# Optimization experiments

Hardware: AMD Instinct MI355X
Metric: run time of the kernel (lower is better)

## Reference

```python
import jax, jax.numpy as jnp
import numpy as np

B = 4096
STATE_DIM = 64
OBS_DIM = 32
BASE_DEGREE = 8
TIME_STEPS = 96
EPS = 1e-7


def _degree(t):
    # get_degree: degree_params initialized to linspace(0,1,time_steps); used via .item() (static)
    p = float(t) / (TIME_STEPS - 1)
    scaled = 0.5 * (1.0 + np.sin(2.0 * np.pi * p))
    return BASE_DEGREE + int(2.0 * scaled)


def _cheby_fwd_and_jac(x, coeffs, degree):
    """ChebyKAN forward y[b,o] = sum_{i,d} coeffs[i,o,d] * cos(d*acos(clip(tanh(x[b,i]))))
    plus its analytic per-sample Jacobian J[b,o,i] (replaces the torch autograd loop)."""
    t_raw = jnp.tanh(x)                                   # [B, D]
    t_val = jnp.clip(t_raw, -1.0 + EPS, 1.0 - EPS)
    theta = jnp.arccos(t_val)                             # [B, D]
    dvals = jnp.arange(degree + 1, dtype=x.dtype)         # [deg+1]
    ang = theta[..., None] * dvals                        # [B, D, deg+1]
    cheb = jnp.cos(ang)
    ac = coeffs[..., : degree + 1]                        # [D, D, deg+1]
    y = jnp.einsum('bid,iod->bo', cheb, ac)               # [B, D]
    # d cheb / d x = d*sin(d*theta) * (1 - tanh(x)^2) * mask / sqrt(1 - t_val^2)
    mask = ((t_raw > -1.0 + EPS) & (t_raw < 1.0 - EPS)).astype(x.dtype)
    dtheta_dx = -(1.0 - t_raw * t_raw) * mask / jnp.sqrt(1.0 - t_val * t_val)  # [B, D]
    dcheb_dx = -dvals * jnp.sin(ang) * dtheta_dx[..., None]                    # [B, D, deg+1]
    jac = jnp.einsum('bid,iod->boi', dcheb_dx, ac)        # [B, D, D] = dY_o/dx_i
    return y, jac


def setup_inputs() -> dict:
    key = jax.random.key(0)
    ks = jax.random.split(key, 5)
    obs = jax.random.normal(ks[0], (B, OBS_DIM), jnp.float32)
    prev_state = jax.random.normal(ks[1], (B, STATE_DIM), jnp.float32)
    A = jax.random.normal(ks[2], (B, STATE_DIM, STATE_DIM), jnp.float32)
    prev_cov = A @ A.transpose(0, 2, 1) / STATE_DIM + jnp.eye(STATE_DIM, dtype=jnp.float32)  # SPD
    bound = 1.0 / np.sqrt(STATE_DIM * (BASE_DEGREE + 3))  # kaiming-uniform style
    coeffs = jax.random.uniform(ks[3], (STATE_DIM, STATE_DIM, BASE_DEGREE + 3), jnp.float32, -bound, bound)
    M = jax.random.normal(ks[4], (STATE_DIM, OBS_DIM), jnp.float32)
    q, _ = jnp.linalg.qr(M)                               # orthonormal columns
    obs_matrix = q.T.astype(jnp.float32)                  # [OBS_DIM, STATE_DIM], orthogonal rows
    log_Q_diag = jnp.zeros((STATE_DIM,), jnp.float32)
    log_R_diag = jnp.zeros((OBS_DIM,), jnp.float32)
    return dict(obs=obs, prev_state=prev_state, prev_cov=prev_cov, coeffs=coeffs,
                obs_matrix=obs_matrix, log_Q_diag=log_Q_diag, log_R_diag=log_R_diag, t=10)


def reference(obs, prev_state, prev_cov, coeffs, obs_matrix, log_Q_diag, log_R_diag, t):
    degree = _degree(t)
    state_pred, Fj = _cheby_fwd_and_jac(prev_state, coeffs, degree)   # [B,D], [B,D,D]
    q = jnp.exp(log_Q_diag)                                           # [D]
    r = jnp.exp(log_R_diag)                                           # [O]
    H = obs_matrix                                                    # [O, D]
    # cov_pred = F P F^T + Q
    cov_pred = jnp.einsum('bij,bjk,blk->bil', Fj, prev_cov, Fj) + jnp.diag(q)[None]
    obs_pred = state_pred @ H.T                                       # [B, O]
    residual = obs - obs_pred                                         # [B, O]
    # S = H Pp H^T + R
    S = jnp.einsum('ij,bjk,lk->bil', H, cov_pred, H) + jnp.diag(r)[None]
    S_inv = jnp.linalg.pinv(S)                                        # [B, O, O]
    PHt = jnp.einsum('bij,oj->bio', cov_pred, H)                      # [B, D, O]
    K = jnp.einsum('bio,bop->bip', PHt, S_inv)                        # [B, D, O]
    state_update = state_pred + jnp.einsum('bio,bo->bi', K, residual)
    I_KH = jnp.eye(STATE_DIM, dtype=cov_pred.dtype)[None] - jnp.einsum('bio,oj->bij', K, H)
    # Joseph form: (I-KH) Pp (I-KH)^T + K R K^T
    cov_update = (jnp.einsum('bij,bjk,blk->bil', I_KH, cov_pred, I_KH)
                  + jnp.einsum('bio,o,bjo->bij', K, r, K))
    cov_diag = jnp.diagonal(cov_update, axis1=1, axis2=2)
    return state_update, cov_update, cov_diag
```

## Files before the change

kernel.cpp:

```cpp
#include <hip/hip_runtime.h>
#include <math.h>


typedef float f4 __attribute__((ext_vector_type(4)));
typedef float f32x4 __attribute__((ext_vector_type(4)));
typedef short b16x8 __attribute__((ext_vector_type(8)));
typedef short b16x4 __attribute__((ext_vector_type(4)));

#define EPSC 1e-7f
#define MFMA(a, b, c) __builtin_amdgcn_mfma_f32_16x16x32_bf16(a, b, c, 0, 0, 0)
static constexpr size_t CU_OFF = 4096 * 64;
static constexpr size_t CD_OFF = CU_OFF + 4096ull * 4096;

__device__ __forceinline__ void split2(float x, short &h, short &l) {
  unsigned u = __float_as_uint(x);
  h = (short)(u >> 16);
  float rem = x - __uint_as_float(u & 0xffff0000u);
  l = (short)(__float_as_uint(rem) >> 16);
}

__device__ __forceinline__ void split8v(f4 a, f4 b, b16x8 &hi, b16x8 &lo) {
#pragma unroll
  for (int j = 0; j < 4; ++j) {
    short hh, ll;
    split2(a[j], hh, ll); hi[j] = hh; lo[j] = ll;
    split2(b[j], hh, ll); hi[4 + j] = hh; lo[4 + j] = ll;
  }
}

__global__ __launch_bounds__(256, 3) void kalman_fused(
    const float *__restrict__ obs, const float *__restrict__ prev_state,
    const float *__restrict__ prev_cov, const float *__restrict__ coeffs,
    const float *__restrict__ Hm, const float *__restrict__ logQ,
    const float *__restrict__ logR, const int *__restrict__ tptr,
    float *__restrict__ out) {
  __shared__ __align__(16) unsigned char pool[43008];
  unsigned short *sPh = (unsigned short *)(pool);
  unsigned short *sPl = (unsigned short *)(pool + 9216);
  unsigned short *sFh = (unsigned short *)(pool + 18432);
  unsigned short *sFl = (unsigned short *)(pool + 27648);
  float *sT = (float *)(pool);
  float *sCov = (float *)(pool + 18432);
  float *sPHt = (float *)(pool);
  float *sK = (float *)(pool + 9216);
  float *sS = (float *)(pool + 36864);
  float *ypart = (float *)(pool + 36864);
  float *sy = (float *)(pool + 41472);
  float *sresid = (float *)(pool + 41728);
  float *sq = (float *)(pool + 41856);
  float *sr = (float *)(pool + 42112);
  float *sTv = (float *)(pool + 42240);
  float *sSn = (float *)(pool + 42496);
  float *sDth = (float *)(pool + 42752);

  const int tid = (int)threadIdx.x;
  const int b = (int)blockIdx.x;
  const int w = tid >> 6;
  const int l = tid & 63;
  const int lr = l & 15;
  const int h = l >> 4;

  const int tval = tptr[0];
  const float ang = 6.28318530717958647f * ((float)tval / 95.0f);
  const int D = 9 + (int)(1.0f + sinf(ang));

  {
    const float *Pg = prev_cov + (size_t)b * 4096;
#pragma unroll
    for (int e = 0; e < 4; ++e) {
      const int idx = tid + 256 * e;
      f4 v = *(const f4 *)(Pg + 4 * idx);
      const int r = idx >> 4, c = (idx & 15) * 4;
      b16x4 h4, l4;
#pragma unroll
      for (int j = 0; j < 4; ++j) {
        short hh, ll;
        split2(v[j], hh, ll);
        h4[j] = hh; l4[j] = ll;
      }
      *(b16x4 *)(sPh + r * 72 + c) = h4;
      *(b16x4 *)(sPl + r * 72 + c) = l4;
    }
    if (tid < 64) {
      sq[tid] = expf(logQ[tid]);
      const float x = prev_state[b * 64 + tid];
      const float tr_ = tanhf(x);
      const float tv = fminf(fmaxf(tr_, -1.0f + EPSC), 1.0f - EPSC);
      const float sn = sqrtf(fmaxf(1.0f - tv * tv, 0.0f));
      const float mask = (tr_ > -1.0f + EPSC && tr_ < 1.0f - EPSC) ? 1.0f : 0.0f;
      sTv[tid] = tv;
      sSn[tid] = sn;
      sDth[tid] = -(1.0f - tr_ * tr_) * mask / sn;
    } else if (tid < 96) {
      sr[tid - 64] = expf(logR[tid - 64]);
    }
  }
  __syncthreads();

  {
    const int o = tid & 63, g = tid >> 6;
    float yacc = 0.f;
    float fr[16];
#pragma unroll
    for (int ii = 0; ii < 16; ++ii) {
      const int i = g * 16 + ii;
      const float tv = sTv[i], sn = sSn[i], dth = sDth[i];
      const float *cp = coeffs + (size_t)(i * 64 + o) * 11;
      float cy[11];
#pragma unroll
      for (int d = 0; d < 11; ++d) cy[d] = cp[d];
      if (D < 10) cy[9] = 0.f;
      if (D < 11) cy[10] = 0.f;
      float yac = fmaf(cy[1], tv, cy[0]);
      float wac = cy[1] * sn;
      float cm2 = 1.f, cm1 = tv, sm2 = 0.f, sm1 = sn;
      const float tv2 = 2.f * tv;
#pragma unroll
      for (int d = 2; d <= 10; ++d) {
        const float cc = fmaf(tv2, cm1, -cm2);
        const float ss = fmaf(tv2, sm1, -sm2);
        yac = fmaf(cy[d], cc, yac);
        wac = fmaf(cy[d] * (float)d, ss, wac);
        cm2 = cm1; cm1 = cc; sm2 = sm1; sm1 = ss;
      }
      yacc += yac;
      fr[ii] = -dth * wac;
    }
    b16x8 fh0, fh1, fl0, fl1;
#pragma unroll
    for (int j = 0; j < 8; ++j) {
      short hh, ll;
      split2(fr[j], hh, ll); fh0[j] = hh; fl0[j] = ll;
      split2(fr[8 + j], hh, ll); fh1[j] = hh; fl1[j] = ll;
    }
    *(b16x8 *)(sFh + o * 72 + g * 16) = fh0;
    *(b16x8 *)(sFh + o * 72 + g * 16 + 8) = fh1;
    *(b16x8 *)(sFl + o * 72 + g * 16) = fl0;
    *(b16x8 *)(sFl + o * 72 + g * 16 + 8) = fl1;
    ypart[g * 64 + o] = yacc;
  }
  __syncthreads();
  if (tid < 64)
    sy[tid] = ypart[tid] + ypart[64 + tid] + ypart[128 + tid] + ypart[192 + tid];
  __syncthreads();

  if (tid < 32) {
    float racc = obs[b * 32 + tid];
    const float *Hr = Hm + tid * 64;
#pragma unroll
    for (int s = 0; s < 64; s += 4) {
      f4 hv = *(const f4 *)(Hr + s);
      racc -= hv[0] * sy[s] + hv[1] * sy[s + 1] + hv[2] * sy[s + 2] +
              hv[3] * sy[s + 3];
    }
    sresid[tid] = racc;
  }

  f32x4 accT[4] = {{0.f, 0.f, 0.f, 0.f}, {0.f, 0.f, 0.f, 0.f},
                   {0.f, 0.f, 0.f, 0.f}, {0.f, 0.f, 0.f, 0.f}};
  {
    const int m = 16 * w + lr;
#pragma unroll
    for (int kc = 0; kc < 2; ++kc) {
      const int k = kc * 32 + h * 8;
      b16x8 Ah = *(const b16x8 *)(sFh + m * 72 + k);
      b16x8 Al = *(const b16x8 *)(sFl + m * 72 + k);
#pragma unroll
      for (int t = 0; t < 4; ++t) {
        const int n = t * 16 + lr;
        b16x8 Bh = *(const b16x8 *)(sPh + n * 72 + k);
        b16x8 Bl = *(const b16x8 *)(sPl + n * 72 + k);
        accT[t] = MFMA(Ah, Bh, accT[t]);
        accT[t] = MFMA(Al, Bh, accT[t]);
        accT[t] = MFMA(Ah, Bl, accT[t]);
      }
    }
  }
  __syncthreads();
  {
    const int r0 = 16 * w + h * 4;
#pragma unroll
    for (int t = 0; t < 4; ++t)
#pragma unroll
      for (int j = 0; j < 4; ++j)
        sT[(r0 + j) * 68 + t * 16 + lr] = accT[t][j];
  }

  f32x4 accC[4] = {{0.f, 0.f, 0.f, 0.f}, {0.f, 0.f, 0.f, 0.f},
                   {0.f, 0.f, 0.f, 0.f}, {0.f, 0.f, 0.f, 0.f}};
  {
    const int m = 16 * w + lr;
#pragma unroll
    for (int kc = 0; kc < 2; ++kc) {
      const int k = kc * 32 + h * 8;
      f4 a0 = *(const f4 *)(sT + m * 68 + k);
      f4 a1 = *(const f4 *)(sT + m * 68 + k + 4);
      b16x8 Ah, Al;
      split8v(a0, a1, Ah, Al);
#pragma unroll
      for (int t = 0; t < 4; ++t) {
        const int n = t * 16 + lr;
        b16x8 Bh = *(const b16x8 *)(sFh + n * 72 + k);
        b16x8 Bl = *(const b16x8 *)(sFl + n * 72 + k);
        accC[t] = MFMA(Ah, Bh, accC[t]);
        accC[t] = MFMA(Al, Bh, accC[t]);
        accC[t] = MFMA(Ah, Bl, accC[t]);
      }
    }
  }
  __syncthreads();
  {
    const int r0 = 16 * w + h * 4;
#pragma unroll
    for (int t = 0; t < 4; ++t)
#pragma unroll
      for (int j = 0; j < 4; ++j) {
        const int rr = r0 + j, cc = t * 16 + lr;
        float v = accC[t][j];
        if (rr == cc) v += sq[rr];
        sCov[rr * 68 + cc] = v;
      }
  }

  {
    f32x4 acc[2] = {{0.f, 0.f, 0.f, 0.f}, {0.f, 0.f, 0.f, 0.f}};
    const int m = 16 * w + lr;
#pragma unroll
    for (int kc = 0; kc < 2; ++kc) {
      const int k = kc * 32 + h * 8;
      f4 a0 = *(const f4 *)(sCov + m * 68 + k);
      f4 a1 = *(const f4 *)(sCov + m * 68 + k + 4);
      b16x8 Ah, Al;
      split8v(a0, a1, Ah, Al);
#pragma unroll
      for (int t = 0; t < 2; ++t) {
        const int n = t * 16 + lr;
        const float *Hr = Hm + n * 64 + k;
        f4 b0 = *(const f4 *)(Hr);
        f4 b1 = *(const f4 *)(Hr + 4);
        b16x8 Bh, Bl;
        split8v(b0, b1, Bh, Bl);
        acc[t] = MFMA(Ah, Bh, acc[t]);
        acc[t] = MFMA(Al, Bh, acc[t]);
        acc[t] = MFMA(Ah, Bl, acc[t]);
      }
    }
    const int r0 = 16 * w + h * 4;
#pragma unroll
    for (int t = 0; t < 2; ++t)
#pragma unroll
      for (int j = 0; j < 4; ++j)
        sPHt[(r0 + j) * 36 + t * 16 + lr] = acc[t][j];
  }
  __syncthreads();

  {
    const int tr = w >> 1, tc = w & 1;
    f32x4 acc = {0.f, 0.f, 0.f, 0.f};
    const int m = tr * 16 + lr;
    const int n = tc * 16 + lr;
#pragma unroll
    for (int kc = 0; kc < 2; ++kc) {
      const int k = kc * 32 + h * 8;
      const float *Hr = Hm + m * 64 + k;
      f4 a0 = *(const f4 *)(Hr);
      f4 a1 = *(const f4 *)(Hr + 4);
      b16x8 Ah, Al;
      split8v(a0, a1, Ah, Al);
      f4 b0, b1;
#pragma unroll
      for (int j = 0; j < 4; ++j) b0[j] = sPHt[(k + j) * 36 + n];
#pragma unroll
      for (int j = 0; j < 4; ++j) b1[j] = sPHt[(k + 4 + j) * 36 + n];
      b16x8 Bh, Bl;
      split8v(b0, b1, Bh, Bl);
      acc = MFMA(Ah, Bh, acc);
      acc = MFMA(Al, Bh, acc);
      acc = MFMA(Ah, Bl, acc);
    }
    const int r0 = tr * 16 + h * 4;
#pragma unroll
    for (int j = 0; j < 4; ++j) {
      const int rr = r0 + j, cc = tc * 16 + lr;
      float v = acc[j];
      if (rr == cc) v += sr[rr];
      sS[rr * 36 + cc] = v;
    }
  }
  __syncthreads();

  if (w == 0) {
    const int mr = l >> 1, half = l & 1;
    float s0[16];
    const float *gbase = sS + mr * 36 + half * 16;
    {
      f4 v0 = *(const f4 *)(gbase + 0), v1 = *(const f4 *)(gbase + 4);
      f4 v2 = *(const f4 *)(gbase + 8), v3 = *(const f4 *)(gbase + 12);
#pragma unroll
      for (int j = 0; j < 4; ++j) {
        s0[j] = v0[j]; s0[4 + j] = v1[j]; s0[8 + j] = v2[j]; s0[12 + j] = v3[j];
      }
    }
#pragma unroll
    for (int p = 0; p < 32; ++p) {
      const int ph = p >> 4, pi = p & 15;
      float prow[16];
#pragma unroll
      for (int j = 0; j < 16; ++j) prow[j] = __shfl(s0[j], 2 * p + half, 64);
      const float dpp = __shfl(s0[pi], 2 * p + ph, 64);
      const float d = 1.0f / dpp;
      const float fv = __shfl(s0[pi], (l & 62) + ph, 64);
      if (mr == p) {
#pragma unroll
        for (int j = 0; j < 16; ++j) s0[j] = prow[j] * d;
        if (half == ph) s0[pi] = d;
      } else {
        const float fd = fv * d;
#pragma unroll
        for (int j = 0; j < 16; ++j) s0[j] = fmaf(-fd, prow[j], s0[j]);
        if (half == ph) s0[pi] = -fd;
      }
    }
    float *wbase = sS + mr * 36 + half * 16;
    f4 w0 = {s0[0], s0[1], s0[2], s0[3]};
    f4 w1 = {s0[4], s0[5], s0[6], s0[7]};
    f4 w2 = {s0[8], s0[9], s0[10], s0[11]};
    f4 w3 = {s0[12], s0[13], s0[14], s0[15]};
    *(f4 *)(wbase + 0) = w0;
    *(f4 *)(wbase + 4) = w1;
    *(f4 *)(wbase + 8) = w2;
    *(f4 *)(wbase + 12) = w3;
  }
  __syncthreads();

  {
    f32x4 acc[2] = {{0.f, 0.f, 0.f, 0.f}, {0.f, 0.f, 0.f, 0.f}};
    const int m = 16 * w + lr;
    const int k = h * 8;
    f4 a0 = *(const f4 *)(sPHt + m * 36 + k);
    f4 a1 = *(const f4 *)(sPHt + m * 36 + k + 4);
    b16x8 Ah, Al;
    split8v(a0, a1, Ah, Al);
#pragma unroll
    for (int t = 0; t < 2; ++t) {
      const int n = t * 16 + lr;
      f4 b0 = *(const f4 *)(sS + n * 36 + k);
      f4 b1 = *(const f4 *)(sS + n * 36 + k + 4);
      b16x8 Bh, Bl;
      split8v(b0, b1, Bh, Bl);
      acc[t] = MFMA(Ah, Bh, acc[t]);
      acc[t] = MFMA(Al, Bh, acc[t]);
      acc[t] = MFMA(Ah, Bl, acc[t]);
    }
    const int r0 = 16 * w + h * 4;
#pragma unroll
    for (int t = 0; t < 2; ++t)
#pragma unroll
      for (int j = 0; j < 4; ++j)
        sK[(r0 + j) * 36 + t * 16 + lr] = acc[t][j];
  }
  __syncthreads();

  if (tid < 64) {
    float su = sy[tid];
#pragma unroll
    for (int ob = 0; ob < 32; ob += 4) {
      f4 kv = *(const f4 *)(sK + tid * 36 + ob);
      su += kv[0] * sresid[ob] + kv[1] * sresid[ob + 1] +
            kv[2] * sresid[ob + 2] + kv[3] * sresid[ob + 3];
    }
    out[b * 64 + tid] = su;
  }
  {
    const int m = 16 * w + lr;
    const int k = h * 8;
    f4 a0 = *(const f4 *)(sK + m * 36 + k);
    f4 a1 = *(const f4 *)(sK + m * 36 + k + 4);
    a0 = -a0;
    a1 = -a1;
    b16x8 Ah, Al;
    split8v(a0, a1, Ah, Al);
    const int r0 = 16 * w + h * 4;
    float *outc = out + CU_OFF + (size_t)b * 4096;
#pragma unroll
    for (int t = 0; t < 4; ++t) {
      const int n = t * 16 + lr;
      f4 b0 = *(const f4 *)(sPHt + n * 36 + k);
      f4 b1 = *(const f4 *)(sPHt + n * 36 + k + 4);
      b16x8 Bh, Bl;
      split8v(b0, b1, Bh, Bl);
      f32x4 acc;
#pragma unroll
      for (int j = 0; j < 4; ++j) acc[j] = sCov[(r0 + j) * 68 + n];
      acc = MFMA(Ah, Bh, acc);
      acc = MFMA(Al, Bh, acc);
      acc = MFMA(Ah, Bl, acc);
#pragma unroll
      for (int j = 0; j < 4; ++j) {
        const int rr = r0 + j;
        outc[rr * 64 + n] = acc[j];
        if (rr == n) out[CD_OFF + b * 64 + rr] = acc[j];
      }
    }
  }
}

extern "C" void kernel_launch(void *const *d_in, const int *in_sizes, int n_in,
                              void *d_out, int out_size, void *d_ws,
                              size_t ws_size, hipStream_t stream) {
  const float *obs = (const float *)d_in[0];
  const float *prev_state = (const float *)d_in[1];
  const float *prev_cov = (const float *)d_in[2];
  const float *coeffs = (const float *)d_in[3];
  const float *Hm = (const float *)d_in[4];
  const float *logQ = (const float *)d_in[5];
  const float *logR = (const float *)d_in[6];
  const int *tptr = (const int *)d_in[7];
  (void)in_sizes; (void)n_in; (void)out_size; (void)d_ws; (void)ws_size;
  kalman_fused<<<dim3(4096), dim3(256), 0, stream>>>(
      obs, prev_state, prev_cov, coeffs, Hm, logQ, logR, tptr, (float *)d_out);
}
```

Baseline: 128.6 us.

## Store intermediates as packed bf16 hi/lo pairs with XOR-swizzled LDS layout

Intermediate matrices (T, cov_pred, PHt, K) are now stored in LDS as packed 32-bit hi|lo bf16 split words, so consumers unpack them with byte-permute instructions instead of re-splitting floats. Padded row strides are replaced by XOR swizzles to avoid bank conflicts, which shrinks LDS use and lets launch bounds ask for 4 blocks per CU instead of 3. Coefficient loads are vectorized into f4 loads. Risks: storing cov_pred as hi+lo bf16 loses a few mantissa bits in the Joseph-form accumulator input, and higher occupancy may force register spills.

```diff
diff --git a/kernel.cpp b/kernel.cpp
--- a/kernel.cpp
+++ b/kernel.cpp
@@ -6,6 +6,9 @@
 typedef float f32x4 __attribute__((ext_vector_type(4)));
 typedef short b16x8 __attribute__((ext_vector_type(8)));
 typedef short b16x4 __attribute__((ext_vector_type(4)));
+typedef unsigned int u32;
+typedef unsigned int u32x4 __attribute__((ext_vector_type(4)));
+typedef unsigned short u16;
 
 #define EPSC 1e-7f
 #define MFMA(a, b, c) __builtin_amdgcn_mfma_f32_16x16x32_bf16(a, b, c, 0, 0, 0)
@@ -13,12 +16,34 @@
 static constexpr size_t CD_OFF = CU_OFF + 4096ull * 4096;
 
 __device__ __forceinline__ void split2(float x, short &h, short &l) {
-  unsigned u = __float_as_uint(x);
+  u32 u = __float_as_uint(x);
   h = (short)(u >> 16);
   float rem = x - __uint_as_float(u & 0xffff0000u);
   l = (short)(__float_as_uint(rem) >> 16);
 }
-
+__device__ __forceinline__ u32 packsplit(float x) {
+  u32 u = __float_as_uint(x) & 0xffff0000u;
+  float rem = x - __uint_as_float(u);
+  return u | (__float_as_uint(rem) >> 16);
+}
+__device__ __forceinline__ float unpackf(u32 v) {
+  return __uint_as_float(v & 0xffff0000u) + __uint_as_float(v << 16);
+}
+union U8 { u32x4 u; b16x8 s; };
+__device__ __forceinline__ void unpack8(u32x4 q0, u32x4 q1, b16x8 &hi,
+                                        b16x8 &lo) {
+  U8 H, L;
+  H.u[0] = __builtin_amdgcn_perm(q0[1], q0[0], 0x07060302u);
+  H.u[1] = __builtin_amdgcn_perm(q0[3], q0[2], 0x07060302u);
+  H.u[2] = __builtin_amdgcn_perm(q1[1], q1[0], 0x07060302u);
+  H.u[3] = __builtin_amdgcn_perm(q1[3], q1[2], 0x07060302u);
+  L.u[0] = __builtin_amdgcn_perm(q0[1], q0[0], 0x05040100u);
+  L.u[1] = __builtin_amdgcn_perm(q0[3], q0[2], 0x05040100u);
+  L.u[2] = __builtin_amdgcn_perm(q1[1], q1[0], 0x05040100u);
+  L.u[3] = __builtin_amdgcn_perm(q1[3], q1[2], 0x05040100u);
+  hi = H.s;
+  lo = L.s;
+}
 __device__ __forceinline__ void split8v(f4 a, f4 b, b16x8 &hi, b16x8 &lo) {
 #pragma unroll
   for (int j = 0; j < 4; ++j) {
@@ -28,30 +53,30 @@
   }
 }
 
-__global__ __launch_bounds__(256, 3) void kalman_fused(
+__global__ __launch_bounds__(256, 4) void kalman_fused(
     const float *__restrict__ obs, const float *__restrict__ prev_state,
     const float *__restrict__ prev_cov, const float *__restrict__ coeffs,
     const float *__restrict__ Hm, const float *__restrict__ logQ,
     const float *__restrict__ logR, const int *__restrict__ tptr,
     float *__restrict__ out) {
-  __shared__ __align__(16) unsigned char pool[43008];
-  unsigned short *sPh = (unsigned short *)(pool);
-  unsigned short *sPl = (unsigned short *)(pool + 9216);
-  unsigned short *sFh = (unsigned short *)(pool + 18432);
-  unsigned short *sFl = (unsigned short *)(pool + 27648);
-  float *sT = (float *)(pool);
-  float *sCov = (float *)(pool + 18432);
-  float *sPHt = (float *)(pool);
-  float *sK = (float *)(pool + 9216);
-  float *sS = (float *)(pool + 36864);
-  float *ypart = (float *)(pool + 36864);
-  float *sy = (float *)(pool + 41472);
-  float *sresid = (float *)(pool + 41728);
-  float *sq = (float *)(pool + 41856);
-  float *sr = (float *)(pool + 42112);
-  float *sTv = (float *)(pool + 42240);
-  float *sSn = (float *)(pool + 42496);
-  float *sDth = (float *)(pool + 42752);
+  __shared__ __align__(16) unsigned char pool[38144];
+  u16 *sPh = (u16 *)(pool);
+  u16 *sPl = (u16 *)(pool + 8192);
+  u32 *sT = (u32 *)(pool);
+  u32 *sPHt = (u32 *)(pool);
+  u32 *sK = (u32 *)(pool + 8192);
+  u16 *sFh = (u16 *)(pool + 16384);
+  u16 *sFl = (u16 *)(pool + 24576);
+  u32 *sCov = (u32 *)(pool + 16384);
+  float *sS = (float *)(pool + 32768);
+  float *ypart = (float *)(pool + 32768);
+  float *sTv = (float *)(pool + 33792);
+  float *sSn = (float *)(pool + 34048);
+  float *sDth = (float *)(pool + 34304);
+  float *sy = (float *)(pool + 37376);
+  float *sresid = (float *)(pool + 37632);
+  float *sq = (float *)(pool + 37760);
+  float *sr = (float *)(pool + 38016);
 
   const int tid = (int)threadIdx.x;
   const int b = (int)blockIdx.x;
@@ -71,6 +96,7 @@
       const int idx = tid + 256 * e;
       f4 v = *(const f4 *)(Pg + 4 * idx);
       const int r = idx >> 4, c = (idx & 15) * 4;
+      const int x = (r & 7) << 3;
       b16x4 h4, l4;
 #pragma unroll
       for (int j = 0; j < 4; ++j) {
@@ -78,13 +104,13 @@
         split2(v[j], hh, ll);
         h4[j] = hh; l4[j] = ll;
       }
-      *(b16x4 *)(sPh + r * 72 + c) = h4;
-      *(b16x4 *)(sPl + r * 72 + c) = l4;
+      *(b16x4 *)(sPh + r * 64 + (c ^ x)) = h4;
+      *(b16x4 *)(sPl + r * 64 + (c ^ x)) = l4;
     }
     if (tid < 64) {
       sq[tid] = expf(logQ[tid]);
-      const float x = prev_state[b * 64 + tid];
-      const float tr_ = tanhf(x);
+      const float xx = prev_state[b * 64 + tid];
+      const float tr_ = tanhf(xx);
       const float tv = fminf(fmaxf(tr_, -1.0f + EPSC), 1.0f - EPSC);
       const float sn = sqrtf(fmaxf(1.0f - tv * tv, 0.0f));
       const float mask = (tr_ > -1.0f + EPSC && tr_ < 1.0f - EPSC) ? 1.0f : 0.0f;
@@ -106,9 +132,13 @@
       const int i = g * 16 + ii;
       const float tv = sTv[i], sn = sSn[i], dth = sDth[i];
       const float *cp = coeffs + (size_t)(i * 64 + o) * 11;
+      f4 q0 = *(const f4 *)(cp);
+      f4 q1 = *(const f4 *)(cp + 4);
+      f4 q2 = *(const f4 *)(cp + 7);
       float cy[11];
 #pragma unroll
-      for (int d = 0; d < 11; ++d) cy[d] = cp[d];
+      for (int j = 0; j < 4; ++j) { cy[j] = q0[j]; cy[4 + j] = q1[j]; }
+      cy[8] = q2[1]; cy[9] = q2[2]; cy[10] = q2[3];
       if (D < 10) cy[9] = 0.f;
       if (D < 11) cy[10] = 0.f;
       float yac = fmaf(cy[1], tv, cy[0]);
@@ -133,10 +163,11 @@
       split2(fr[j], hh, ll); fh0[j] = hh; fl0[j] = ll;
       split2(fr[8 + j], hh, ll); fh1[j] = hh; fl1[j] = ll;
     }
-    *(b16x8 *)(sFh + o * 72 + g * 16) = fh0;
-    *(b16x8 *)(sFh + o * 72 + g * 16 + 8) = fh1;
-    *(b16x8 *)(sFl + o * 72 + g * 16) = fl0;
-    *(b16x8 *)(sFl + o * 72 + g * 16 + 8) = fl1;
+    const int x = (o & 7) << 3;
+    *(b16x8 *)(sFh + o * 64 + ((g * 16) ^ x)) = fh0;
+    *(b16x8 *)(sFh + o * 64 + ((g * 16 + 8) ^ x)) = fh1;
+    *(b16x8 *)(sFl + o * 64 + ((g * 16) ^ x)) = fl0;
+    *(b16x8 *)(sFl + o * 64 + ((g * 16 + 8) ^ x)) = fl1;
     ypart[g * 64 + o] = yacc;
   }
   __syncthreads();
@@ -160,16 +191,18 @@
                    {0.f, 0.f, 0.f, 0.f}, {0.f, 0.f, 0.f, 0.f}};
   {
     const int m = 16 * w + lr;
+    const int xA = (m & 7) << 3;
 #pragma unroll
     for (int kc = 0; kc < 2; ++kc) {
       const int k = kc * 32 + h * 8;
-      b16x8 Ah = *(const b16x8 *)(sFh + m * 72 + k);
-      b16x8 Al = *(const b16x8 *)(sFl + m * 72 + k);
+      b16x8 Ah = *(const b16x8 *)(sFh + m * 64 + (k ^ xA));
+      b16x8 Al = *(const b16x8 *)(sFl + m * 64 + (k ^ xA));
 #pragma unroll
       for (int t = 0; t < 4; ++t) {
         const int n = t * 16 + lr;
-        b16x8 Bh = *(const b16x8 *)(sPh + n * 72 + k);
-        b16x8 Bl = *(const b16x8 *)(sPl + n * 72 + k);
+        const int xB = (n & 7) << 3;
+        b16x8 Bh = *(const b16x8 *)(sPh + n * 64 + (k ^ xB));
+        b16x8 Bl = *(const b16x8 *)(sPl + n * 64 + (k ^ xB));
         accT[t] = MFMA(Ah, Bh, accT[t]);
         accT[t] = MFMA(Al, Bh, accT[t]);
         accT[t] = MFMA(Ah, Bl, accT[t]);
@@ -182,26 +215,31 @@
 #pragma unroll
     for (int t = 0; t < 4; ++t)
 #pragma unroll
-      for (int j = 0; j < 4; ++j)
-        sT[(r0 + j) * 68 + t * 16 + lr] = accT[t][j];
+      for (int j = 0; j < 4; ++j) {
+        const int rr = r0 + j, cc = t * 16 + lr;
+        sT[rr * 64 + (cc ^ ((rr & 7) << 2))] = packsplit(accT[t][j]);
+      }
   }
 
   f32x4 accC[4] = {{0.f, 0.f, 0.f, 0.f}, {0.f, 0.f, 0.f, 0.f},
                    {0.f, 0.f, 0.f, 0.f}, {0.f, 0.f, 0.f, 0.f}};
   {
     const int m = 16 * w + lr;
+    const int xA = (m & 7) << 2;
+    const u32 *Tb = sT + m * 64;
 #pragma unroll
     for (int kc = 0; kc < 2; ++kc) {
       const int k = kc * 32 + h * 8;
-      f4 a0 = *(const f4 *)(sT + m * 68 + k);
-      f4 a1 = *(const f4 *)(sT + m * 68 + k + 4);
+      u32x4 q0 = *(const u32x4 *)(Tb + (k ^ xA));
+      u32x4 q1 = *(const u32x4 *)(Tb + ((k + 4) ^ xA));
       b16x8 Ah, Al;
-      split8v(a0, a1, Ah, Al);
+      unpack8(q0, q1, Ah, Al);
 #pragma unroll
       for (int t = 0; t < 4; ++t) {
         const int n = t * 16 + lr;
-        b16x8 Bh = *(const b16x8 *)(sFh + n * 72 + k);
-        b16x8 Bl = *(const b16x8 *)(sFl + n * 72 + k);
+        const int xB = (n & 7) << 3;
+        b16x8 Bh = *(const b16x8 *)(sFh + n * 64 + (k ^ xB));
+        b16x8 Bl = *(const b16x8 *)(sFl + n * 64 + (k ^ xB));
         accC[t] = MFMA(Ah, Bh, accC[t]);
         accC[t] = MFMA(Al, Bh, accC[t]);
         accC[t] = MFMA(Ah, Bl, accC[t]);
@@ -218,20 +256,22 @@
         const int rr = r0 + j, cc = t * 16 + lr;
         float v = accC[t][j];
         if (rr == cc) v += sq[rr];
-        sCov[rr * 68 + cc] = v;
+        sCov[rr * 64 + (cc ^ ((rr & 7) << 2))] = packsplit(v);
       }
   }
 
   {
     f32x4 acc[2] = {{0.f, 0.f, 0.f, 0.f}, {0.f, 0.f, 0.f, 0.f}};
     const int m = 16 * w + lr;
+    const int xA = (m & 7) << 2;
+    const u32 *Cb = sCov + m * 64;
 #pragma unroll
     for (int kc = 0; kc < 2; ++kc) {
       const int k = kc * 32 + h * 8;
-      f4 a0 = *(const f4 *)(sCov + m * 68 + k);
-      f4 a1 = *(const f4 *)(sCov + m * 68 + k + 4);
+      u32x4 q0 = *(const u32x4 *)(Cb + (k ^ xA));
+      u32x4 q1 = *(const u32x4 *)(Cb + ((k + 4) ^ xA));
       b16x8 Ah, Al;
-      split8v(a0, a1, Ah, Al);
+      unpack8(q0, q1, Ah, Al);
 #pragma unroll
       for (int t = 0; t < 2; ++t) {
         const int n = t * 16 + lr;
@@ -249,8 +289,10 @@
 #pragma unroll
     for (int t = 0; t < 2; ++t)
 #pragma unroll
-      for (int j = 0; j < 4; ++j)
-        sPHt[(r0 + j) * 36 + t * 16 + lr] = acc[t][j];
+      for (int j = 0; j < 4; ++j) {
+        const int rr = r0 + j, cc = t * 16 + lr;
+        sPHt[rr * 32 + (cc ^ ((rr & 7) << 2))] = packsplit(acc[t][j]);
+      }
   }
   __syncthreads();
 
@@ -267,13 +309,15 @@
       f4 a1 = *(const f4 *)(Hr + 4);
       b16x8 Ah, Al;
       split8v(a0, a1, Ah, Al);
-      f4 b0, b1;
-#pragma unroll
-      for (int j = 0; j < 4; ++j) b0[j] = sPHt[(k + j) * 36 + n];
-#pragma unroll
-      for (int j = 0; j < 4; ++j) b1[j] = sPHt[(k + 4 + j) * 36 + n];
+      u32x4 q0, q1;
+#pragma unroll
+      for (int j = 0; j < 4; ++j)
+        q0[j] = sPHt[(k + j) * 32 + (n ^ (j << 2))];
+#pragma unroll
+      for (int j = 0; j < 4; ++j)
+        q1[j] = sPHt[(k + 4 + j) * 32 + (n ^ ((4 + j) << 2))];
       b16x8 Bh, Bl;
-      split8v(b0, b1, Bh, Bl);
+      unpack8(q0, q1, Bh, Bl);
       acc = MFMA(Ah, Bh, acc);
       acc = MFMA(Al, Bh, acc);
       acc = MFMA(Ah, Bl, acc);
@@ -336,11 +380,12 @@
   {
     f32x4 acc[2] = {{0.f, 0.f, 0.f, 0.f}, {0.f, 0.f, 0.f, 0.f}};
     const int m = 16 * w + lr;
+    const int xA = (m & 7) << 2;
     const int k = h * 8;
-    f4 a0 = *(const f4 *)(sPHt + m * 36 + k);
-    f4 a1 = *(const f4 *)(sPHt + m * 36 + k + 4);
+    u32x4 q0 = *(const u32x4 *)(sPHt + m * 32 + (k ^ xA));
+    u32x4 q1 = *(const u32x4 *)(sPHt + m * 32 + ((k + 4) ^ xA));
     b16x8 Ah, Al;
-    split8v(a0, a1, Ah, Al);
+    unpack8(q0, q1, Ah, Al);
 #pragma unroll
     for (int t = 0; t < 2; ++t) {
       const int n = t * 16 + lr;
@@ -356,42 +401,55 @@
 #pragma unroll
     for (int t = 0; t < 2; ++t)
 #pragma unroll
-      for (int j = 0; j < 4; ++j)
-        sK[(r0 + j) * 36 + t * 16 + lr] = acc[t][j];
+      for (int j = 0; j < 4; ++j) {
+        const int rr = r0 + j, cc = t * 16 + lr;
+        sK[rr * 32 + (cc ^ ((rr & 7) << 2))] = packsplit(acc[t][j]);
+      }
   }
   __syncthreads();
 
   if (tid < 64) {
     float su = sy[tid];
-#pragma unroll
-    for (int ob = 0; ob < 32; ob += 4) {
-      f4 kv = *(const f4 *)(sK + tid * 36 + ob);
-      su += kv[0] * sresid[ob] + kv[1] * sresid[ob + 1] +
-            kv[2] * sresid[ob + 2] + kv[3] * sresid[ob + 3];
+    const int x = (tid & 7) << 2;
+    const u32 *Kb = sK + tid * 32;
+#pragma unroll
+    for (int c0 = 0; c0 < 32; c0 += 4) {
+      u32x4 q = *(const u32x4 *)(Kb + (c0 ^ x));
+#pragma unroll
+      for (int j = 0; j < 4; ++j)
+        su = fmaf(unpackf(q[j]), sresid[c0 + j], su);
     }
     out[b * 64 + tid] = su;
   }
   {
     const int m = 16 * w + lr;
+    const int xA = (m & 7) << 2;
     const int k = h * 8;
-    f4 a0 = *(const f4 *)(sK + m * 36 + k);
-    f4 a1 = *(const f4 *)(sK + m * 36 + k + 4);
-    a0 = -a0;
-    a1 = -a1;
+    u32x4 q0 = *(const u32x4 *)(sK + m * 32 + (k ^ xA));
+    u32x4 q1 = *(const u32x4 *)(sK + m * 32 + ((k + 4) ^ xA));
+#pragma unroll
+    for (int j = 0; j < 4; ++j) {
+      q0[j] ^= 0x80008000u;
+      q1[j] ^= 0x80008000u;
+    }
     b16x8 Ah, Al;
-    split8v(a0, a1, Ah, Al);
+    unpack8(q0, q1, Ah, Al);
     const int r0 = 16 * w + h * 4;
     float *outc = out + CU_OFF + (size_t)b * 4096;
 #pragma unroll
     for (int t = 0; t < 4; ++t) {
       const int n = t * 16 + lr;
-      f4 b0 = *(const f4 *)(sPHt + n * 36 + k);
-      f4 b1 = *(const f4 *)(sPHt + n * 36 + k + 4);
+      const int xB = (n & 7) << 2;
+      u32x4 p0 = *(const u32x4 *)(sPHt + n * 32 + (k ^ xB));
+      u32x4 p1 = *(const u32x4 *)(sPHt + n * 32 + ((k + 4) ^ xB));
       b16x8 Bh, Bl;
-      split8v(b0, b1, Bh, Bl);
+      unpack8(p0, p1, Bh, Bl);
       f32x4 acc;
 #pragma unroll
-      for (int j = 0; j < 4; ++j) acc[j] = sCov[(r0 + j) * 68 + n];
+      for (int j = 0; j < 4; ++j) {
+        const int rr = r0 + j;
+        acc[j] = unpackf(sCov[rr * 64 + (n ^ ((rr & 7) << 2))]);
+      }
       acc = MFMA(Ah, Bh, acc);
       acc = MFMA(Al, Bh, acc);
       acc = MFMA(Ah, Bl, acc);
```

Result: faster. 115.8 us (median of 2 runs) (-10.0%).
